# Kernel tuning notes

Hardware: AMD Instinct MI355X
Metric: run time of the kernel (lower is better)

Reference implementation:

```python
import jax, jax.numpy as jnp
import numpy as np

S, B, T, A = 512, 64, 768, 512
H1 = (T + T) // 2   # 768
H2 = (T + A) // 2   # 640


def setup_inputs() -> dict:
    key = jax.random.key(0)
    ks = jax.random.split(key, 11)
    sc = 0.02
    return {
        "text": jax.random.normal(ks[0], (B, T), jnp.float32),
        "anp": jax.random.normal(ks[1], (B, A), jnp.float32),
        "text_seq": jax.random.normal(ks[2], (S, B, T), jnp.float32),
        "W11": jax.random.normal(ks[3], (2 * T, H1), jnp.float32) * sc,
        "b11": jax.random.normal(ks[4], (H1,), jnp.float32) * sc,
        "W21": jax.random.normal(ks[5], (H1, 1), jnp.float32) * sc,
        "b21": jax.random.normal(ks[6], (1,), jnp.float32) * sc,
        "W12": jax.random.normal(ks[7], (T + A, H2), jnp.float32) * sc,
        "b12": jax.random.normal(ks[8], (H2,), jnp.float32) * sc,
        "W22": jax.random.normal(ks[9], (H2, 1), jnp.float32) * sc,
        "b22": jax.random.normal(ks[10], (1,), jnp.float32) * sc,
    }


def reference(text, anp, text_seq, W11, b11, W21, b21, W12, b12, W22, b22):
    t = text_seq.shape[-1]
    # cat([text_seq[i], text]) @ W11 == text_seq @ W11[:t] + text @ W11[t:]
    h1 = jnp.tanh(jnp.einsum("sbt,th->sbh", text_seq, W11[:t]) + text @ W11[t:] + b11)
    h2 = jnp.tanh(jnp.einsum("sbt,th->sbh", text_seq, W12[:t]) + anp @ W12[t:] + b12)
    s1 = h1 @ W21 + b21            # (S, B, 1)
    s2 = h2 @ W22 + b22            # (S, B, 1)
    w1 = jax.nn.softmax(s1, axis=0)
    w2 = jax.nn.softmax(s2, axis=0)
    return jnp.mean((w1 + w2) * text_seq * 0.5, axis=0)  # (B, T)
```

## Files before the change

kernel.cpp:

```cpp
#include <hip/hip_runtime.h>
#include <stdint.h>

#define S_DIM 512
#define B_DIM 64
#define T_DIM 768
#define A_DIM 512
#define H1_DIM 768
#define H2_DIM 640
#define N_DIM (H1_DIM + H2_DIM)
#define M_DIM (S_DIM * B_DIM)
#define K_DIM T_DIM
#define NSLOT 22

typedef short s16x8 __attribute__((ext_vector_type(8)));
typedef float f32x4 __attribute__((ext_vector_type(4)));

__device__ __forceinline__ unsigned short f2bf(float f) {
    unsigned u = __float_as_uint(f);
    u += 0x7fffu + ((u >> 16) & 1u);
    return (unsigned short)(u >> 16);
}

#define CONVA_BLKS (M_DIM * K_DIM / 1024)
#define CONVW_BLKS (N_DIM * K_DIM / 256)

__global__ __launch_bounds__(256) void prep_kernel(const float* __restrict__ ts,
                                                   const float* __restrict__ W11,
                                                   const float* __restrict__ W12,
                                                   unsigned short* __restrict__ Abf,
                                                   unsigned short* __restrict__ Bt) {
    const int blk = blockIdx.x;
    if (blk < CONVA_BLKS) {
        int i = blk * 256 + threadIdx.x;
        float4 v = ((const float4*)ts)[i];
        ushort4 o;
        o.x = f2bf(v.x); o.y = f2bf(v.y); o.z = f2bf(v.z); o.w = f2bf(v.w);
        ((ushort4*)Abf)[i] = o;
    } else {
        int e = (blk - CONVA_BLKS) * 256 + threadIdx.x;
        int n = e / K_DIM, k = e % K_DIM;
        float v = (n < H1_DIM) ? W11[k * H1_DIM + n] : W12[k * H2_DIM + (n - H1_DIM)];
        Bt[e] = f2bf(v);
    }
}

__global__ __launch_bounds__(256) void bias_kernel(const float* __restrict__ text,
                                                   const float* __restrict__ anp,
                                                   const float* __restrict__ W11,
                                                   const float* __restrict__ b11,
                                                   const float* __restrict__ W12,
                                                   const float* __restrict__ b12,
                                                   float* __restrict__ cbias) {
    const int chunk = blockIdx.x;
    const int b     = blockIdx.y;
    const int nl    = threadIdx.x & 63;
    const int kg    = threadIdx.x >> 6;
    __shared__ float red[256];
    float a0 = 0.f, a1 = 0.f;
    if (chunk < 12) {
        const int n = chunk * 64 + nl;
        const float* w = W11 + (size_t)T_DIM * H1_DIM + n;
        const float* x = text + b * T_DIM;
        for (int k = kg; k < T_DIM; k += 8) {
            a0 = fmaf(x[k],     w[(size_t)k * H1_DIM],       a0);
            a1 = fmaf(x[k + 4], w[(size_t)(k + 4) * H1_DIM], a1);
        }
    } else {
        const int n2 = (chunk - 12) * 64 + nl;
        const float* w = W12 + (size_t)T_DIM * H2_DIM + n2;
        const float* x = anp + b * A_DIM;
        for (int k = kg; k < A_DIM; k += 8) {
            a0 = fmaf(x[k],     w[(size_t)k * H2_DIM],       a0);
            a1 = fmaf(x[k + 4], w[(size_t)(k + 4) * H2_DIM], a1);
        }
    }
    red[kg * 64 + nl] = a0 + a1;
    __syncthreads();
    if (kg == 0) {
        const int n = chunk < 12 ? chunk * 64 + nl : H1_DIM + (chunk - 12) * 64 + nl;
        float base = (chunk < 12) ? b11[n] : b12[n - H1_DIM];
        cbias[b * N_DIM + n] =
            base + ((red[nl] + red[64 + nl]) + (red[128 + nl] + red[192 + nl]));
    }
}

#define BM 128
#define BN 128
#define BK 64

__global__ __launch_bounds__(256, 3) void gemm_score_kernel(
        const unsigned short* __restrict__ A,
        const unsigned short* __restrict__ Bt,
        const float* __restrict__ cbias,
        const float* __restrict__ W21,
        const float* __restrict__ W22,
        float* __restrict__ part) {
    __shared__ __align__(16) unsigned short As[BM * BK];
    __shared__ __align__(16) unsigned short Bs[BN * BK];
    const int tid  = threadIdx.x;
    const int m0   = blockIdx.x * BM;
    const int n0   = blockIdx.y * BN;
    const int lane = tid & 63;
    const int wave = tid >> 6;
    const int wm   = wave & 1;
    const int wn   = wave >> 1;
    const int quad = lane >> 4;
    const int col  = lane & 15;
    const int cswz = col & 7;

    f32x4 acc[4][4] = {};

    const int wrow = lane >> 3;
    const int kof  = (((lane & 7) ^ wrow) & 7) * 8;

    for (int k0 = 0; k0 < K_DIM; k0 += BK) {
        #pragma unroll
        for (int p = 0; p < 4; ++p) {
            const int r0 = p * 32 + wave * 8;
            __builtin_amdgcn_global_load_lds(
                (__attribute__((address_space(1))) void*)&A[(size_t)(m0 + r0 + wrow) * K_DIM + k0 + kof],
                (__attribute__((address_space(3))) void*)&As[r0 * BK],
                16, 0, 0);
            __builtin_amdgcn_global_load_lds(
                (__attribute__((address_space(1))) void*)&Bt[(size_t)(n0 + r0 + wrow) * K_DIM + k0 + kof],
                (__attribute__((address_space(3))) void*)&Bs[r0 * BK],
                16, 0, 0);
        }
        __syncthreads();
        #pragma unroll
        for (int kk = 0; kk < BK; kk += 32) {
            s16x8 af[4], bf[4];
            const int ch = ((kk >> 3) + quad) ^ cswz;
            #pragma unroll
            for (int i = 0; i < 4; ++i)
                af[i] = *(const s16x8*)&As[(wm * 64 + i * 16 + col) * BK + ch * 8];
            #pragma unroll
            for (int j = 0; j < 4; ++j)
                bf[j] = *(const s16x8*)&Bs[(wn * 64 + j * 16 + col) * BK + ch * 8];
            #pragma unroll
            for (int i = 0; i < 4; ++i)
                #pragma unroll
                for (int j = 0; j < 4; ++j)
                    acc[i][j] = __builtin_amdgcn_mfma_f32_16x16x32_bf16(af[i], bf[j], acc[i][j], 0, 0, 0);
        }
        __syncthreads();
    }

    const int half = (n0 >= H1_DIM) ? 1 : 0;
    const int jb   = n0 >> 7;
    const float* w2p = half ? (W22 - H1_DIM) : W21;
    int   ncol[4];
    float w2v[4];
    #pragma unroll
    for (int j = 0; j < 4; ++j) {
        ncol[j] = n0 + wn * 64 + j * 16 + col;
        w2v[j]  = w2p[ncol[j]];
    }
    float* pc = part + (jb * 2 + wn) * M_DIM;
    #pragma unroll
    for (int i = 0; i < 4; ++i) {
        #pragma unroll
        for (int r = 0; r < 4; ++r) {
            int row_local = wm * 64 + i * 16 + quad * 4 + r;
            int b = row_local & (B_DIM - 1);
            int s = (m0 + row_local) >> 6;
            float v = 0.f;
            #pragma unroll
            for (int j = 0; j < 4; ++j) {
                float pre = acc[i][j][r] + cbias[b * N_DIM + ncol[j]];
                float ex  = __expf(2.f * pre);
                float th  = 1.f - 2.f * __builtin_amdgcn_rcpf(ex + 1.f);
                v = fmaf(th, w2v[j], v);
            }
            v += __shfl_xor(v, 1);
            v += __shfl_xor(v, 2);
            v += __shfl_xor(v, 4);
            v += __shfl_xor(v, 8);
            if (col == 0) pc[b * S_DIM + s] = v;
        }
    }
}

__global__ __launch_bounds__(512) void softmax_kernel(const float* __restrict__ part,
                                                      float* __restrict__ wsum) {
    const int b = blockIdx.x, s = threadIdx.x;
    __shared__ float redm[16], reds[16];
    float v0 = 0.f, v1 = 0.f;
    #pragma unroll
    for (int sl = 0; sl < 12; ++sl)       v0 += part[sl * M_DIM + b * S_DIM + s];
    #pragma unroll
    for (int sl = 12; sl < NSLOT; ++sl)   v1 += part[sl * M_DIM + b * S_DIM + s];
    float m0 = v0, m1 = v1;
    #pragma unroll
    for (int off = 32; off > 0; off >>= 1) {
        m0 = fmaxf(m0, __shfl_xor(m0, off));
        m1 = fmaxf(m1, __shfl_xor(m1, off));
    }
    const int w = s >> 6;
    if ((s & 63) == 0) { redm[w] = m0; redm[8 + w] = m1; }
    __syncthreads();
    m0 = redm[0]; m1 = redm[8];
    #pragma unroll
    for (int i = 1; i < 8; ++i) { m0 = fmaxf(m0, redm[i]); m1 = fmaxf(m1, redm[8 + i]); }
    float e0 = expf(v0 - m0), e1 = expf(v1 - m1);
    float s0 = e0, s1 = e1;
    #pragma unroll
    for (int off = 32; off > 0; off >>= 1) {
        s0 += __shfl_xor(s0, off);
        s1 += __shfl_xor(s1, off);
    }
    if ((s & 63) == 0) { reds[w] = s0; reds[8 + w] = s1; }
    __syncthreads();
    s0 = reds[0]; s1 = reds[8];
    #pragma unroll
    for (int i = 1; i < 8; ++i) { s0 += reds[i]; s1 += reds[8 + i]; }
    wsum[b * S_DIM + s] = e0 / s0 + e1 / s1;
}

__global__ __launch_bounds__(128) void wmean_kernel(const unsigned short* __restrict__ Abf,
                                                    const float* __restrict__ wsum,
                                                    float* __restrict__ out) {
    const int b  = blockIdx.x;
    const int tp = blockIdx.y * 128 + threadIdx.x;
    const unsigned short* base = Abf + (size_t)b * T_DIM + tp * 2;
    const float* wp = wsum + b * S_DIM;
    float a0 = 0.f, a1 = 0.f, c0 = 0.f, c1 = 0.f;
    #pragma unroll 4
    for (int s = 0; s < S_DIM; s += 2) {
        float w0 = wp[s], w1 = wp[s + 1];
        unsigned u0 = *(const unsigned*)(base + (size_t)s * (B_DIM * T_DIM));
        unsigned u1 = *(const unsigned*)(base + (size_t)(s + 1) * (B_DIM * T_DIM));
        a0 = fmaf(w0, __uint_as_float(u0 << 16),          a0);
        a1 = fmaf(w0, __uint_as_float(u0 & 0xffff0000u),  a1);
        c0 = fmaf(w1, __uint_as_float(u1 << 16),          c0);
        c1 = fmaf(w1, __uint_as_float(u1 & 0xffff0000u),  c1);
    }
    out[b * T_DIM + tp * 2]     = (a0 + c0) * (0.5f / (float)S_DIM);
    out[b * T_DIM + tp * 2 + 1] = (a1 + c1) * (0.5f / (float)S_DIM);
}

extern "C" void kernel_launch(void* const* d_in, const int* in_sizes, int n_in,
                              void* d_out, int out_size, void* d_ws, size_t ws_size,
                              hipStream_t stream) {
    const float* text = (const float*)d_in[0];
    const float* anp  = (const float*)d_in[1];
    const float* ts   = (const float*)d_in[2];
    const float* W11  = (const float*)d_in[3];
    const float* b11  = (const float*)d_in[4];
    const float* W21  = (const float*)d_in[5];
    const float* W12  = (const float*)d_in[7];
    const float* b12  = (const float*)d_in[8];
    const float* W22  = (const float*)d_in[9];
    float* out = (float*)d_out;

    char* ws = (char*)d_ws;
    unsigned short* Abf = (unsigned short*)ws;
    unsigned short* Bt  = (unsigned short*)(ws + 50331648);
    float* cbias = (float*)(ws + 50331648 + 2162688);
    float* part  = (float*)(ws + 50331648 + 2162688 + 360448);
    float* wsum  = (float*)(ws + 50331648 + 2162688 + 360448 + 2883584);

    prep_kernel<<<CONVA_BLKS + CONVW_BLKS, 256, 0, stream>>>(ts, W11, W12, Abf, Bt);
    bias_kernel<<<dim3(22, B_DIM), 256, 0, stream>>>(text, anp, W11, b11, W12, b12, cbias);
    gemm_score_kernel<<<dim3(M_DIM / BM, N_DIM / BN), 256, 0, stream>>>(
        Abf, Bt, cbias, W21, W22, part);
    softmax_kernel<<<B_DIM, 512, 0, stream>>>(part, wsum);
    wmean_kernel<<<dim3(B_DIM, 3), 128, 0, stream>>>(Abf, wsum, out);
}
```

Before: 337.9 us.

## Merge bias into prep kernel, remap GEMM blocks per XCD, split wmean over S

The bias projection kernel is folded into the prep kernel as extra blocks, which saves one launch. The GEMM grid becomes 1D with a mapping that sends eight consecutive M tiles, one per XCD, to share the same N tile, aiming for better L2 reuse of tiles. The weighted-mean kernel is split four ways along S to raise parallelism over its original 192 blocks, and the partial sums are combined with float atomics into an output zeroed by a memset. This adds the memset, atomic traffic and order-dependent summation.

```diff
diff --git a/kernel.cpp b/kernel.cpp
--- a/kernel.cpp
+++ b/kernel.cpp
@@ -23,64 +23,63 @@
 
 #define CONVA_BLKS (M_DIM * K_DIM / 1024)
 #define CONVW_BLKS (N_DIM * K_DIM / 256)
+#define BIAS_BLKS  (22 * B_DIM)
 
 __global__ __launch_bounds__(256) void prep_kernel(const float* __restrict__ ts,
+                                                   const float* __restrict__ text,
+                                                   const float* __restrict__ anp,
                                                    const float* __restrict__ W11,
+                                                   const float* __restrict__ b11,
                                                    const float* __restrict__ W12,
+                                                   const float* __restrict__ b12,
                                                    unsigned short* __restrict__ Abf,
-                                                   unsigned short* __restrict__ Bt) {
+                                                   unsigned short* __restrict__ Bt,
+                                                   float* __restrict__ cbias) {
     const int blk = blockIdx.x;
+    __shared__ float red[256];
     if (blk < CONVA_BLKS) {
         int i = blk * 256 + threadIdx.x;
         float4 v = ((const float4*)ts)[i];
         ushort4 o;
         o.x = f2bf(v.x); o.y = f2bf(v.y); o.z = f2bf(v.z); o.w = f2bf(v.w);
         ((ushort4*)Abf)[i] = o;
-    } else {
+    } else if (blk < CONVA_BLKS + CONVW_BLKS) {
         int e = (blk - CONVA_BLKS) * 256 + threadIdx.x;
         int n = e / K_DIM, k = e % K_DIM;
         float v = (n < H1_DIM) ? W11[k * H1_DIM + n] : W12[k * H2_DIM + (n - H1_DIM)];
         Bt[e] = f2bf(v);
-    }
-}
-
-__global__ __launch_bounds__(256) void bias_kernel(const float* __restrict__ text,
-                                                   const float* __restrict__ anp,
-                                                   const float* __restrict__ W11,
-                                                   const float* __restrict__ b11,
-                                                   const float* __restrict__ W12,
-                                                   const float* __restrict__ b12,
-                                                   float* __restrict__ cbias) {
-    const int chunk = blockIdx.x;
-    const int b     = blockIdx.y;
-    const int nl    = threadIdx.x & 63;
-    const int kg    = threadIdx.x >> 6;
-    __shared__ float red[256];
-    float a0 = 0.f, a1 = 0.f;
-    if (chunk < 12) {
-        const int n = chunk * 64 + nl;
-        const float* w = W11 + (size_t)T_DIM * H1_DIM + n;
-        const float* x = text + b * T_DIM;
-        for (int k = kg; k < T_DIM; k += 8) {
-            a0 = fmaf(x[k],     w[(size_t)k * H1_DIM],       a0);
-            a1 = fmaf(x[k + 4], w[(size_t)(k + 4) * H1_DIM], a1);
-        }
     } else {
-        const int n2 = (chunk - 12) * 64 + nl;
-        const float* w = W12 + (size_t)T_DIM * H2_DIM + n2;
-        const float* x = anp + b * A_DIM;
-        for (int k = kg; k < A_DIM; k += 8) {
-            a0 = fmaf(x[k],     w[(size_t)k * H2_DIM],       a0);
-            a1 = fmaf(x[k + 4], w[(size_t)(k + 4) * H2_DIM], a1);
-        }
-    }
-    red[kg * 64 + nl] = a0 + a1;
-    __syncthreads();
-    if (kg == 0) {
-        const int n = chunk < 12 ? chunk * 64 + nl : H1_DIM + (chunk - 12) * 64 + nl;
-        float base = (chunk < 12) ? b11[n] : b12[n - H1_DIM];
-        cbias[b * N_DIM + n] =
-            base + ((red[nl] + red[64 + nl]) + (red[128 + nl] + red[192 + nl]));
+        const int t     = blk - CONVA_BLKS - CONVW_BLKS;
+        const int chunk = t % 22;
+        const int b     = t / 22;
+        const int nl    = threadIdx.x & 63;
+        const int kg    = threadIdx.x >> 6;
+        float a0 = 0.f, a1 = 0.f;
+        if (chunk < 12) {
+            const int n = chunk * 64 + nl;
+            const float* w = W11 + (size_t)T_DIM * H1_DIM + n;
+            const float* x = text + b * T_DIM;
+            for (int k = kg; k < T_DIM; k += 8) {
+                a0 = fmaf(x[k],     w[(size_t)k * H1_DIM],       a0);
+                a1 = fmaf(x[k + 4], w[(size_t)(k + 4) * H1_DIM], a1);
+            }
+        } else {
+            const int n2 = (chunk - 12) * 64 + nl;
+            const float* w = W12 + (size_t)T_DIM * H2_DIM + n2;
+            const float* x = anp + b * A_DIM;
+            for (int k = kg; k < A_DIM; k += 8) {
+                a0 = fmaf(x[k],     w[(size_t)k * H2_DIM],       a0);
+                a1 = fmaf(x[k + 4], w[(size_t)(k + 4) * H2_DIM], a1);
+            }
+        }
+        red[kg * 64 + nl] = a0 + a1;
+        __syncthreads();
+        if (kg == 0) {
+            const int n = chunk < 12 ? chunk * 64 + nl : H1_DIM + (chunk - 12) * 64 + nl;
+            float base = (chunk < 12) ? b11[n] : b12[n - H1_DIM];
+            cbias[b * N_DIM + n] =
+                base + ((red[nl] + red[64 + nl]) + (red[128 + nl] + red[192 + nl]));
+        }
     }
 }
 
@@ -98,8 +97,11 @@
     __shared__ __align__(16) unsigned short As[BM * BK];
     __shared__ __align__(16) unsigned short Bs[BN * BK];
     const int tid  = threadIdx.x;
-    const int m0   = blockIdx.x * BM;
-    const int n0   = blockIdx.y * BN;
+    const int lb   = blockIdx.x;
+    const int xcd  = lb & 7;
+    const int ib   = lb >> 3;
+    const int m0   = ((ib / 11) * 8 + xcd) * BM;
+    const int n0   = (ib % 11) * BN;
     const int lane = tid & 63;
     const int wave = tid >> 6;
     const int wm   = wave & 1;
@@ -222,11 +224,12 @@
                                                     float* __restrict__ out) {
     const int b  = blockIdx.x;
     const int tp = blockIdx.y * 128 + threadIdx.x;
+    const int s0 = blockIdx.z * 128;
     const unsigned short* base = Abf + (size_t)b * T_DIM + tp * 2;
     const float* wp = wsum + b * S_DIM;
     float a0 = 0.f, a1 = 0.f, c0 = 0.f, c1 = 0.f;
     #pragma unroll 4
-    for (int s = 0; s < S_DIM; s += 2) {
+    for (int s = s0; s < s0 + 128; s += 2) {
         float w0 = wp[s], w1 = wp[s + 1];
         unsigned u0 = *(const unsigned*)(base + (size_t)s * (B_DIM * T_DIM));
         unsigned u1 = *(const unsigned*)(base + (size_t)(s + 1) * (B_DIM * T_DIM));
@@ -235,8 +238,8 @@
         c0 = fmaf(w1, __uint_as_float(u1 << 16),          c0);
         c1 = fmaf(w1, __uint_as_float(u1 & 0xffff0000u),  c1);
     }
-    out[b * T_DIM + tp * 2]     = (a0 + c0) * (0.5f / (float)S_DIM);
-    out[b * T_DIM + tp * 2 + 1] = (a1 + c1) * (0.5f / (float)S_DIM);
+    atomicAdd(&out[b * T_DIM + tp * 2],     (a0 + c0) * (0.5f / (float)S_DIM));
+    atomicAdd(&out[b * T_DIM + tp * 2 + 1], (a1 + c1) * (0.5f / (float)S_DIM));
 }
 
 extern "C" void kernel_launch(void* const* d_in, const int* in_sizes, int n_in,
@@ -260,10 +263,11 @@
     float* part  = (float*)(ws + 50331648 + 2162688 + 360448);
     float* wsum  = (float*)(ws + 50331648 + 2162688 + 360448 + 2883584);
 
-    prep_kernel<<<CONVA_BLKS + CONVW_BLKS, 256, 0, stream>>>(ts, W11, W12, Abf, Bt);
-    bias_kernel<<<dim3(22, B_DIM), 256, 0, stream>>>(text, anp, W11, b11, W12, b12, cbias);
-    gemm_score_kernel<<<dim3(M_DIM / BM, N_DIM / BN), 256, 0, stream>>>(
+    hipMemsetAsync(out, 0, B_DIM * T_DIM * sizeof(float), stream);
+    prep_kernel<<<CONVA_BLKS + CONVW_BLKS + BIAS_BLKS, 256, 0, stream>>>(
+        ts, text, anp, W11, b11, W12, b12, Abf, Bt, cbias);
+    gemm_score_kernel<<<(M_DIM / BM) * (N_DIM / BN), 256, 0, stream>>>(
         Abf, Bt, cbias, W21, W22, part);
     softmax_kernel<<<B_DIM, 512, 0, stream>>>(part, wsum);
-    wmean_kernel<<<dim3(B_DIM, 3), 128, 0, stream>>>(Abf, wsum, out);
-}
+    wmean_kernel<<<dim3(B_DIM, 3, 4), 128, 0, stream>>>(Abf, wsum, out);
+}
```

Result: faster. 312.7 us (-7.5%).
